# Kernel optimization log

Measured on AMD Instinct MI355X. Metric: run time of the kernel, lower is better.

Reference implementation:

```python
import jax, jax.numpy as jnp
import numpy as np

N = 50000      # nodes
E = 800000     # edges (before self loops)
D_IN = 128
HID = 64
HEADS = 8
D_OUT = 10


def setup_inputs() -> dict:
    key = jax.random.key(0)
    ks = jax.random.split(key, 16)
    sc = 0.05
    x = jax.random.normal(ks[0], (N, D_IN), dtype=jnp.float32)
    edge_index = jax.random.randint(ks[1], (2, E), 0, N, dtype=jnp.int64)
    return {
        "x": x,
        "edge_index": edge_index,
        "W1": jax.random.normal(ks[2], (HEADS * HID, D_IN), dtype=jnp.float32) * sc,
        "a1_src": jax.random.normal(ks[3], (HEADS, HID), dtype=jnp.float32) * sc,
        "a1_dst": jax.random.normal(ks[4], (HEADS, HID), dtype=jnp.float32) * sc,
        "b1": jnp.zeros((HEADS * HID,), jnp.float32),
        "W2": jax.random.normal(ks[5], (HID, HEADS * HID), dtype=jnp.float32) * sc,
        "a2_src": jax.random.normal(ks[6], (1, HID), dtype=jnp.float32) * sc,
        "a2_dst": jax.random.normal(ks[7], (1, HID), dtype=jnp.float32) * sc,
        "b2": jnp.zeros((HID,), jnp.float32),
        "W3": jax.random.normal(ks[8], (HID, HID), dtype=jnp.float32) * sc,
        "a3_src": jax.random.normal(ks[9], (1, HID), dtype=jnp.float32) * sc,
        "a3_dst": jax.random.normal(ks[10], (1, HID), dtype=jnp.float32) * sc,
        "b3": jnp.zeros((HID,), jnp.float32),
        "Wc": jax.random.normal(ks[11], (D_OUT, HID), dtype=jnp.float32) * sc,
        "bc": jnp.zeros((D_OUT,), jnp.float32),
    }


def gat_conv(x, src, dst, W, a_src, a_dst, b, concat):
    """PyG GATConv (eval mode, add_self_loops already applied to src/dst)."""
    heads, out_ch = a_src.shape
    n = x.shape[0]
    h = (x @ W.T).reshape(n, heads, out_ch)          # [N, H, C]
    a_s = jnp.einsum('nhc,hc->nh', h, a_src)          # [N, H]
    a_d = jnp.einsum('nhc,hc->nh', h, a_dst)          # [N, H]
    e = jax.nn.leaky_relu(a_s[src] + a_d[dst], 0.2)   # [Etot, H]
    # segment softmax over incoming edges of each destination node
    m = jax.ops.segment_max(e, dst, num_segments=n)
    ex = jnp.exp(e - m[dst])
    s = jax.ops.segment_sum(ex, dst, num_segments=n)
    alpha = ex / (s[dst] + 1e-16)                     # [Etot, H]
    out = jax.ops.segment_sum(h[src] * alpha[:, :, None], dst, num_segments=n)
    if concat:
        out = out.reshape(n, heads * out_ch)
    else:
        out = out.mean(axis=1)
    return out + b


def reference(x, edge_index, W1, a1_src, a1_dst, b1, W2, a2_src, a2_dst, b2,
              W3, a3_src, a3_dst, b3, Wc, bc):
    loops = jnp.arange(N, dtype=edge_index.dtype)
    src = jnp.concatenate([edge_index[0], loops])
    dst = jnp.concatenate([edge_index[1], loops])
    h = jax.nn.elu(gat_conv(x, src, dst, W1, a1_src, a1_dst, b1, True))
    h = jax.nn.elu(gat_conv(h, src, dst, W2, a2_src, a2_dst, b2, False))
    h = jax.nn.elu(gat_conv(h, src, dst, W3, a3_src, a3_dst, b3, False))
    return h @ Wc.T + bc
```

## Files before the change

### kernel.cpp

```cpp
#include <hip/hip_runtime.h>
#include <math.h>

#define N_NODES 50000
#define N_EDGES 800000
#define ETOT    (N_EDGES + N_NODES)
#define COL_CAP (ETOT + 3 * N_NODES + 64)

typedef short bf16x8 __attribute__((ext_vector_type(8)));
typedef float f32x4  __attribute__((ext_vector_type(4)));
typedef float f32x2  __attribute__((ext_vector_type(2)));

__device__ __forceinline__ float b2f(unsigned int u16) {
    return __uint_as_float(u16 << 16);
}
__device__ __forceinline__ unsigned short f2b(float f) {
    unsigned int u = __float_as_uint(f);
    u += 0x7fffu + ((u >> 16) & 1u);
    return (unsigned short)(u >> 16);
}

__global__ __launch_bounds__(256) void k_prep(const float* __restrict__ x,
                                              const float* __restrict__ w1,
                                              const float* __restrict__ w2,
                                              const float* __restrict__ w3,
                                              const float* __restrict__ a1s,
                                              const float* __restrict__ a1d,
                                              unsigned short* __restrict__ xb,
                                              unsigned short* __restrict__ o1,
                                              unsigned short* __restrict__ o2,
                                              unsigned short* __restrict__ o3,
                                              float* __restrict__ U,
                                              int* __restrict__ deg,
                                              int* __restrict__ flag) {
    int i = blockIdx.x * 256 + threadIdx.x;
    if (i < N_NODES) deg[i] = 0;
    if (i == 0) *flag = 0;
    if (blockIdx.x < 8) {
        int h = blockIdx.x;
        int which = threadIdx.x >> 7, k = threadIdx.x & 127;
        const float* av = which ? a1d : a1s;
        float acc = 0.f;
        for (int c = 0; c < 64; ++c)
            acc += av[h * 64 + c] * w1[(size_t)(h * 64 + c) * 128 + k];
        U[(which * 8 + h) * 128 + k] = acc;
    }
    if (i < 512 * 128 / 4) {
        float4 v = ((const float4*)w1)[i];
        ushort2* o = (ushort2*)(o1 + i * 4);
        o[0] = make_ushort2(f2b(v.x), f2b(v.y));
        o[1] = make_ushort2(f2b(v.z), f2b(v.w));
    }
    if (i < 64 * 512 / 4) {
        float4 v = ((const float4*)w2)[i];
        ushort2* o = (ushort2*)(o2 + i * 4);
        o[0] = make_ushort2(f2b(v.x), f2b(v.y));
        o[1] = make_ushort2(f2b(v.z), f2b(v.w));
    }
    if (i < 64 * 64 / 4) {
        float4 v = ((const float4*)w3)[i];
        ushort2* o = (ushort2*)(o3 + i * 4);
        o[0] = make_ushort2(f2b(v.x), f2b(v.y));
        o[1] = make_ushort2(f2b(v.z), f2b(v.w));
    }
    if (i < N_NODES * 128 / 8) {
        const float4* xp = (const float4*)x + (size_t)i * 2;
        float4 v0 = xp[0], v1 = xp[1];
        unsigned int u0 = (unsigned int)f2b(v0.x) | ((unsigned int)f2b(v0.y) << 16);
        unsigned int u1 = (unsigned int)f2b(v0.z) | ((unsigned int)f2b(v0.w) << 16);
        unsigned int u2 = (unsigned int)f2b(v1.x) | ((unsigned int)f2b(v1.y) << 16);
        unsigned int u3 = (unsigned int)f2b(v1.z) | ((unsigned int)f2b(v1.w) << 16);
        *(uint4*)(xb + (size_t)i * 8) = make_uint4(u0, u1, u2, u3);
    }
}

__global__ __launch_bounds__(256) void k_attn(const unsigned short* __restrict__ xb,
                                              const float* __restrict__ U,
                                              float* __restrict__ asrc,
                                              float* __restrict__ adst) {
    __shared__ float sU[16 * 132];
    __shared__ unsigned short sX[16 * 136];
    int t = threadIdx.x;
    for (int i = t; i < 2048; i += 256) sU[(i >> 7) * 132 + (i & 127)] = U[i];
    int n0 = blockIdx.x * 16;
    {
        int r = t >> 4, c = (t & 15) * 8;
        *(uint4*)&sX[r * 136 + c] = *(const uint4*)(xb + (size_t)(n0 + r) * 128 + c);
    }
    __syncthreads();
    int nl = t >> 4, o = t & 15;
    const unsigned short* xr = sX + nl * 136;
    const float* ur = sU + o * 132;
    float acc = 0.f;
#pragma unroll 8
    for (int k2 = 0; k2 < 128; ++k2) acc += b2f(xr[k2]) * ur[k2];
    int n = n0 + nl;
    if (o < 8) asrc[n * 8 + o] = acc;
    else       adst[n * 8 + (o - 8)] = acc;
}

__global__ void k_detect(const int* __restrict__ idx, int* __restrict__ flag) {
    int i = blockIdx.x * blockDim.x + threadIdx.x;
    int v = idx[2 * i + 1];
    unsigned long long any = __ballot(v != 0);
    if ((threadIdx.x & 63) == 0 && any) atomicOr(flag, 1);
}

__device__ __forceinline__ int edge_src(const int* idx, int e, int is32) {
    return is32 ? idx[e] : idx[2 * e];
}
__device__ __forceinline__ int edge_dst(const int* idx, int e, int is32) {
    return is32 ? idx[N_EDGES + e] : idx[2 * (N_EDGES + e)];
}

__global__ void k_degree(const int* __restrict__ idx, const int* __restrict__ flag,
                         int* __restrict__ deg) {
    int e = blockIdx.x * blockDim.x + threadIdx.x;
    if (e >= ETOT) return;
    int is32 = *flag;
    int d = (e < N_EDGES) ? edge_dst(idx, e, is32) : (e - N_EDGES);
    atomicAdd(&deg[d], 1);
}

__global__ __launch_bounds__(256) void k_scan1(const int* __restrict__ deg,
                                               int* __restrict__ rowptr,
                                               int* __restrict__ bsum) {
    __shared__ int sd[256];
    int t = threadIdx.x;
    int i = blockIdx.x * 256 + t;
    int v = (i < N_NODES) ? ((deg[i] + 3) & ~3) : 0;
    sd[t] = v;
    __syncthreads();
#pragma unroll
    for (int off = 1; off < 256; off <<= 1) {
        int a = (t >= off) ? sd[t - off] : 0;
        __syncthreads();
        sd[t] += a;
        __syncthreads();
    }
    if (i < N_NODES) rowptr[i] = sd[t] - v;
    if (t == 255) bsum[blockIdx.x] = sd[255];
}

__global__ __launch_bounds__(256) void k_scan2(int* __restrict__ bsum,
                                               int* __restrict__ boff,
                                               int* __restrict__ rowptr,
                                               int nb) {
    __shared__ int sd[256];
    int t = threadIdx.x;
    int v = (t < nb) ? bsum[t] : 0;
    sd[t] = v;
    __syncthreads();
#pragma unroll
    for (int off = 1; off < 256; off <<= 1) {
        int a = (t >= off) ? sd[t - off] : 0;
        __syncthreads();
        sd[t] += a;
        __syncthreads();
    }
    boff[t] = sd[t] - v;
    if (t == 255) rowptr[N_NODES] = sd[255];
}

__global__ __launch_bounds__(256) void k_scan3(int* __restrict__ rowptr,
                                               const int* __restrict__ boff,
                                               const int* __restrict__ deg,
                                               int* __restrict__ cursor,
                                               int* __restrict__ col) {
    int i = blockIdx.x * 256 + threadIdx.x;
    if (i == 0) {
        int tot = rowptr[N_NODES];
        for (int q = 0; q < 48; ++q) col[tot + q] = 0;
    }
    if (i >= N_NODES) return;
    int r = rowptr[i] + boff[blockIdx.x];
    rowptr[i] = r;
    cursor[i] = r;
    int d = deg[i];
    int pd = (d + 3) & ~3;
    for (int p = r + d; p < r + pd; ++p) col[p] = 0;
}

__global__ void k_scatter(const int* __restrict__ idx, const int* __restrict__ flag,
                          int* __restrict__ cursor, int* __restrict__ col) {
    int e = blockIdx.x * blockDim.x + threadIdx.x;
    if (e >= ETOT) return;
    int is32 = *flag;
    int s, d;
    if (e < N_EDGES) { s = edge_src(idx, e, is32); d = edge_dst(idx, e, is32); }
    else             { s = d = e - N_EDGES; }
    int pos = atomicAdd(&cursor[d], 1);
    col[pos] = s;
}

__device__ __forceinline__ void aggx_slot(int idx, int rem, float tt, unsigned int xx,
                                          float adn, float& ssum, f32x2* acc) {
    float e = tt + adn;
    e = fmaxf(e, 0.2f * e);
    float ex = __expf(e);
    ex = (idx < rem) ? ex : 0.f;
    ssum += ex;
    float fx = __uint_as_float(xx << 16);
    float fy = __uint_as_float(xx & 0xffff0000u);
    int exi = __float_as_int(ex);
#pragma unroll
    for (int hh = 0; hh < 8; ++hh) {
        float wh = __int_as_float(__builtin_amdgcn_readlane(exi, hh << 3));
        acc[hh].x = fmaf(fx, wh, acc[hh].x);
        acc[hh].y = fmaf(fy, wh, acc[hh].y);
    }
}

__global__ __launch_bounds__(256) void k_aggx(const unsigned short* __restrict__ xb,
                                              const float* __restrict__ asrc,
                                              const float* __restrict__ adst,
                                              const int* __restrict__ rowptr,
                                              const int* __restrict__ degv,
                                              const int* __restrict__ col,
                                              unsigned short* __restrict__ aggX) {
    int n = blockIdx.x * 4 + (threadIdx.x >> 6);
    if (n >= N_NODES) return;
    int l = threadIdx.x & 63;
    int j = l >> 3;
    unsigned lx2 = (unsigned)(l << 1);
    int start = rowptr[n];
    int end   = start + degv[n];
    float adn = adst[((unsigned)n << 3) + (unsigned)j];

    float ssum = 0.f;
    f32x2 acc[8];
#pragma unroll
    for (int hh = 0; hh < 8; ++hh) acc[hh] = (f32x2){0.f, 0.f};

    float tA0, tA1, tA2, tA3, tB0, tB1, tB2, tB3;
    unsigned int xA0, xA1, xA2, xA3, xB0, xB1, xB2, xB3;
    int4 cA, cB;

#define GATHX(c, T0, T1, T2, T3, X0, X1, X2, X3)                              \
    T0 = asrc[(((unsigned)(c).x) << 3) + (unsigned)j];                        \
    T1 = asrc[(((unsigned)(c).y) << 3) + (unsigned)j];                        \
    T2 = asrc[(((unsigned)(c).z) << 3) + (unsigned)j];                        \
    T3 = asrc[(((unsigned)(c).w) << 3) + (unsigned)j];                        \
    X0 = *(const unsigned int*)(xb + (((unsigned)(c).x) << 7) + lx2);         \
    X1 = *(const unsigned int*)(xb + (((unsigned)(c).y) << 7) + lx2);         \
    X2 = *(const unsigned int*)(xb + (((unsigned)(c).z) << 7) + lx2);         \
    X3 = *(const unsigned int*)(xb + (((unsigned)(c).w) << 7) + lx2);

    int k = start;
    cA = *(const int4*)(col + k);
    cB = *(const int4*)(col + k + 4);
    GATHX(cA, tA0, tA1, tA2, tA3, xA0, xA1, xA2, xA3);
    for (;;) {
        bool hasB = (k + 4 < end);
        if (hasB) {
            GATHX(cB, tB0, tB1, tB2, tB3, xB0, xB1, xB2, xB3);
            cA = *(const int4*)(col + k + 8);
        }
        {
            int rem = end - k;
            aggx_slot(0, rem, tA0, xA0, adn, ssum, acc);
            aggx_slot(1, rem, tA1, xA1, adn, ssum, acc);
            aggx_slot(2, rem, tA2, xA2, adn, ssum, acc);
            aggx_slot(3, rem, tA3, xA3, adn, ssum, acc);
        }
        k += 4;
        if (!hasB) break;
        bool hasA = (k + 4 < end);
        if (hasA) {
            GATHX(cA, tA0, tA1, tA2, tA3, xA0, xA1, xA2, xA3);
            cB = *(const int4*)(col + k + 8);
        }
        {
            int rem = end - k;
            aggx_slot(0, rem, tB0, xB0, adn, ssum, acc);
            aggx_slot(1, rem, tB1, xB1, adn, ssum, acc);
            aggx_slot(2, rem, tB2, xB2, adn, ssum, acc);
            aggx_slot(3, rem, tB3, xB3, adn, ssum, acc);
        }
        k += 4;
        if (!hasA) break;
    }
#undef GATHX

    size_t base = (size_t)n * 1024 + lx2;
#pragma unroll
    for (int hh = 0; hh < 8; ++hh) {
        float sh = __int_as_float(__builtin_amdgcn_readlane(__float_as_int(ssum), hh << 3));
        float iv = 1.f / (sh + 1e-16f);
        unsigned int lo = f2b(acc[hh].x * iv);
        unsigned int hi = f2b(acc[hh].y * iv);
        *(unsigned int*)(aggX + base + hh * 128) = lo | (hi << 16);
    }
}

__global__ __launch_bounds__(512, 4) void k_gemm12(const unsigned short* __restrict__ aggX,
                                                   const unsigned short* __restrict__ W1b,
                                                   const float* __restrict__ b1,
                                                   const unsigned short* __restrict__ W2b,
                                                   const float* __restrict__ a2s,
                                                   const float* __restrict__ a2d,
                                                   unsigned short* __restrict__ h2,
                                                   float* __restrict__ asb,
                                                   float* __restrict__ adb) {
    __shared__ unsigned short X2s[64 * 520];
    __shared__ float red_s[8][16];
    __shared__ float red_d[8][16];
    int t = threadIdx.x;
    int w = t >> 6, l = t & 63;
    int quad = l >> 4, lm = l & 15;
    int m0 = blockIdx.x * 64;

    {
        int h = w;
        f32x4 acc1[4][4];
#pragma unroll
        for (int rt = 0; rt < 4; ++rt)
#pragma unroll
            for (int ct = 0; ct < 4; ++ct) acc1[rt][ct] = (f32x4){0.f, 0.f, 0.f, 0.f};

#pragma unroll
        for (int k0 = 0; k0 < 4; ++k0) {
            bf16x8 af[4];
#pragma unroll
            for (int rt = 0; rt < 4; ++rt) {
                int m = m0 + rt * 16 + lm;
                uint4 au = make_uint4(0, 0, 0, 0);
                if (m < N_NODES)
                    au = *(const uint4*)(aggX + (size_t)m * 1024 + h * 128 + k0 * 32 + quad * 8);
                af[rt] = *(bf16x8*)&au;
            }
#pragma unroll
            for (int ct = 0; ct < 4; ++ct) {
                uint4 bu = *(const uint4*)(W1b + (size_t)(h * 64 + ct * 16 + lm) * 128 + k0 * 32 + quad * 8);
                bf16x8 bf_ = *(bf16x8*)&bu;
#pragma unroll
                for (int rt = 0; rt < 4; ++rt)
                    acc1[rt][ct] = __builtin_amdgcn_mfma_f32_16x16x32_bf16(af[rt], bf_, acc1[rt][ct], 0, 0, 0);
            }
        }
#pragma unroll
        for (int ct = 0; ct < 4; ++ct) {
            float bcol = b1[h * 64 + ct * 16 + lm];
#pragma unroll
            for (int rt = 0; rt < 4; ++rt)
#pragma unroll
                for (int g = 0; g < 4; ++g) {
                    float v = acc1[rt][ct][g] + bcol;
                    v = (v > 0.f) ? v : expm1f(v);
                    X2s[(rt * 16 + quad * 4 + g) * 520 + h * 64 + ct * 16 + lm] = f2b(v);
                }
        }
    }
    __syncthreads();

    int rt2 = w >> 1;
    int ct0 = (w & 1) * 2, ct1 = ct0 + 1;
    f32x4 acc2a = (f32x4){0.f, 0.f, 0.f, 0.f};
    f32x4 acc2b = (f32x4){0.f, 0.f, 0.f, 0.f};
#pragma unroll 4
    for (int k0 = 0; k0 < 512; k0 += 32) {
        bf16x8 af = *(const bf16x8*)&X2s[(rt2 * 16 + lm) * 520 + k0 + quad * 8];
        uint4 b0 = *(const uint4*)(W2b + (size_t)(ct0 * 16 + lm) * 512 + k0 + quad * 8);
        uint4 b1u = *(const uint4*)(W2b + (size_t)(ct1 * 16 + lm) * 512 + k0 + quad * 8);
        acc2a = __builtin_amdgcn_mfma_f32_16x16x32_bf16(af, *(bf16x8*)&b0, acc2a, 0, 0, 0);
        acc2b = __builtin_amdgcn_mfma_f32_16x16x32_bf16(af, *(bf16x8*)&b1u, acc2b, 0, 0, 0);
    }

#pragma unroll
    for (int g = 0; g < 4; ++g) {
        int m = m0 + rt2 * 16 + quad * 4 + g;
        if (m < N_NODES) {
            h2[(size_t)m * 64 + ct0 * 16 + lm] = f2b(acc2a[g]);
            h2[(size_t)m * 64 + ct1 * 16 + lm] = f2b(acc2b[g]);
        }
    }

    {
        float as0 = a2s[ct0 * 16 + lm], ad0 = a2d[ct0 * 16 + lm];
        float as1 = a2s[ct1 * 16 + lm], ad1 = a2d[ct1 * 16 + lm];
#pragma unroll
        for (int g = 0; g < 4; ++g) {
            float vs = acc2a[g] * as0 + acc2b[g] * as1;
            float vd = acc2a[g] * ad0 + acc2b[g] * ad1;
#pragma unroll
            for (int off = 1; off < 16; off <<= 1) {
                vs += __shfl_xor(vs, off);
                vd += __shfl_xor(vd, off);
            }
            if (lm == 0) {
                red_s[w][quad * 4 + g] = vs;
                red_d[w][quad * 4 + g] = vd;
            }
        }
    }
    __syncthreads();
    if (t < 64) {
        int rt = t >> 4, rr = t & 15;
        float vs = red_s[2 * rt][rr] + red_s[2 * rt + 1][rr];
        float vd = red_d[2 * rt][rr] + red_d[2 * rt + 1][rr];
        int m = m0 + t;
        if (m < N_NODES) {
            asb[m] = vs;
            adb[m] = vd;
        }
    }
}

__global__ __launch_bounds__(256) void k_gemm(const unsigned short* __restrict__ Ab,
                                              const unsigned short* __restrict__ W,
                                              unsigned short* __restrict__ C,
                                              const float* __restrict__ a_src,
                                              const float* __restrict__ a_dst,
                                              float* __restrict__ asb,
                                              float* __restrict__ adb,
                                              int M, int K, int Nout) {
    __shared__ unsigned short As[64 * 40];
    __shared__ unsigned short Bs[64 * 40];
    __shared__ float red_s[4][64];
    __shared__ float red_d[4][64];
    int t = threadIdx.x;
    int w = t >> 6, l = t & 63;
    int quad = l >> 4, lm = l & 15;
    int m0 = blockIdx.y * 64, n0 = blockIdx.x * 64;
    int lr = t >> 2;
    int lc = (t & 3) * 8;

    f32x4 acc[4];
#pragma unroll
    for (int r = 0; r < 4; ++r) acc[r] = (f32x4){0.f, 0.f, 0.f, 0.f};

    for (int k0 = 0; k0 < K; k0 += 32) {
        int m = m0 + lr;
        uint4 av = make_uint4(0, 0, 0, 0);
        if (m < M) av = *(const uint4*)(Ab + (size_t)m * K + k0 + lc);
        *(uint4*)&As[lr * 40 + lc] = av;
        uint4 bv = *(const uint4*)(W + (size_t)(n0 + lr) * K + k0 + lc);
        *(uint4*)&Bs[lr * 40 + lc] = bv;
        __syncthreads();

        bf16x8 bfrag = *(const bf16x8*)&Bs[(w * 16 + lm) * 40 + quad * 8];
#pragma unroll
        for (int r = 0; r < 4; ++r) {
            bf16x8 afrag = *(const bf16x8*)&As[(r * 16 + lm) * 40 + quad * 8];
            acc[r] = __builtin_amdgcn_mfma_f32_16x16x32_bf16(afrag, bfrag, acc[r], 0, 0, 0);
        }
        __syncthreads();
    }

#pragma unroll
    for (int r = 0; r < 4; ++r)
#pragma unroll
        for (int g = 0; g < 4; ++g) {
            int m = m0 + r * 16 + quad * 4 + g;
            if (m < M) C[(size_t)m * Nout + n0 + w * 16 + lm] = f2b(acc[r][g]);
        }

    float as = a_src[w * 16 + lm];
    float ad = a_dst[w * 16 + lm];
#pragma unroll
    for (int r = 0; r < 4; ++r) {
#pragma unroll
        for (int g = 0; g < 4; ++g) {
            float vs = acc[r][g] * as;
            float vd = acc[r][g] * ad;
#pragma unroll
            for (int off = 1; off < 16; off <<= 1) {
                vs += __shfl_xor(vs, off);
                vd += __shfl_xor(vd, off);
            }
            if (lm == 0) {
                red_s[w][r * 16 + quad * 4 + g] = vs;
                red_d[w][r * 16 + quad * 4 + g] = vd;
            }
        }
    }
    __syncthreads();
    if (t < 64) {
        float vs = red_s[0][t] + red_s[1][t] + red_s[2][t] + red_s[3][t];
        float vd = red_d[0][t] + red_d[1][t] + red_d[2][t] + red_d[3][t];
        int m = m0 + t;
        if (m < M) {
            asb[m] = vs;
            adb[m] = vd;
        }
    }
}

__global__ __launch_bounds__(256) void k_agg1(const unsigned short* __restrict__ h,
                                              const float* __restrict__ asrc,
                                              const float* __restrict__ adst,
                                              const int* __restrict__ rowptr,
                                              const int* __restrict__ degv,
                                              const int* __restrict__ col,
                                              const float* __restrict__ bias,
                                              unsigned short* __restrict__ out) {
    int n = blockIdx.x * 4 + (threadIdx.x >> 6);
    if (n >= N_NODES) return;
    int l = threadIdx.x & 63;
    int start = rowptr[n];
    int end   = start + degv[n];
    float adn = adst[n];

    float ssum = 0.f, o = 0.f;
    float tA0, tA1, tA2, tA3, tB0, tB1, tB2, tB3;
    unsigned short qA0, qA1, qA2, qA3, qB0, qB1, qB2, qB3;
    int4 cA, cB;

#define GATH1(c, T0, T1, T2, T3, Q0, Q1, Q2, Q3)                              \
    T0 = asrc[(unsigned)(c).x];                                               \
    T1 = asrc[(unsigned)(c).y];                                               \
    T2 = asrc[(unsigned)(c).z];                                               \
    T3 = asrc[(unsigned)(c).w];                                               \
    Q0 = h[(((unsigned)(c).x) << 6) + (unsigned)l];                           \
    Q1 = h[(((unsigned)(c).y) << 6) + (unsigned)l];                           \
    Q2 = h[(((unsigned)(c).z) << 6) + (unsigned)l];                           \
    Q3 = h[(((unsigned)(c).w) << 6) + (unsigned)l];

#define ASLOT1(IDX, TT, QQ, rem)                                              \
    {                                                                         \
        float e = TT + adn;                                                   \
        e = fmaxf(e, 0.2f * e);                                               \
        float ex = __expf(e);                                                 \
        ex = ((IDX) < (rem)) ? ex : 0.f;                                      \
        ssum += ex;                                                           \
        o += ex * b2f(QQ);                                                    \
    }

    int k = start;
    cA = *(const int4*)(col + k);
    cB = *(const int4*)(col + k + 4);
    GATH1(cA, tA0, tA1, tA2, tA3, qA0, qA1, qA2, qA3);
    for (;;) {
        bool hasB = (k + 4 < end);
        if (hasB) {
            GATH1(cB, tB0, tB1, tB2, tB3, qB0, qB1, qB2, qB3);
            cA = *(const int4*)(col + k + 8);
        }
        {
            int rem = end - k;
            ASLOT1(0, tA0, qA0, rem);
            ASLOT1(1, tA1, qA1, rem);
            ASLOT1(2, tA2, qA2, rem);
            ASLOT1(3, tA3, qA3, rem);
        }
        k += 4;
        if (!hasB) break;
        bool hasA = (k + 4 < end);
        if (hasA) {
            GATH1(cA, tA0, tA1, tA2, tA3, qA0, qA1, qA2, qA3);
            cB = *(const int4*)(col + k + 8);
        }
        {
            int rem = end - k;
            ASLOT1(0, tB0, qB0, rem);
            ASLOT1(1, tB1, qB1, rem);
            ASLOT1(2, tB2, qB2, rem);
            ASLOT1(3, tB3, qB3, rem);
        }
        k += 4;
        if (!hasA) break;
    }
#undef GATH1
#undef ASLOT1

    float v = o / (ssum + 1e-16f) + bias[l];
    v = (v > 0.f) ? v : expm1f(v);
    out[(size_t)n * 64 + l] = f2b(v);
}

__global__ __launch_bounds__(256) void k_classifier(const unsigned short* __restrict__ h,
                                                    const float* __restrict__ Wc,
                                                    const float* __restrict__ bc,
                                                    float* __restrict__ out) {
    __shared__ float sW[640];
    for (int i = threadIdx.x; i < 640; i += blockDim.x) sW[i] = Wc[i];
    __syncthreads();
    int idx = blockIdx.x * blockDim.x + threadIdx.x;
    if (idx >= N_NODES * 10) return;
    int n = idx / 10, d = idx - n * 10;
    const unsigned short* hr = h + (size_t)n * 64;
    const float* wr = sW + d * 64;
    float acc = 0.f;
#pragma unroll
    for (int c = 0; c < 64; ++c) acc += b2f(hr[c]) * wr[c];
    out[idx] = acc + bc[d];
}

extern "C" void kernel_launch(void* const* d_in, const int* in_sizes, int n_in,
                              void* d_out, int out_size, void* d_ws, size_t ws_size,
                              hipStream_t stream) {
    const float* x    = (const float*)d_in[0];
    const int*   eidx = (const int*)  d_in[1];
    const float* W1   = (const float*)d_in[2];
    const float* a1s  = (const float*)d_in[3];
    const float* a1d  = (const float*)d_in[4];
    const float* b1   = (const float*)d_in[5];
    const float* W2   = (const float*)d_in[6];
    const float* a2s  = (const float*)d_in[7];
    const float* a2d  = (const float*)d_in[8];
    const float* b2   = (const float*)d_in[9];
    const float* W3   = (const float*)d_in[10];
    const float* a3s  = (const float*)d_in[11];
    const float* a3d  = (const float*)d_in[12];
    const float* b3   = (const float*)d_in[13];
    const float* Wc   = (const float*)d_in[14];
    const float* bc   = (const float*)d_in[15];
    float* out = (float*)d_out;

    float* asbuf = (float*)d_ws;
    float* adbuf = asbuf + (size_t)N_NODES * 8;
    unsigned short* aggX = (unsigned short*)(adbuf + (size_t)N_NODES * 8);
    unsigned short* h2  = aggX + (size_t)N_NODES * 1024;
    unsigned short* x3  = h2  + (size_t)N_NODES * 64;
    unsigned short* h3  = x3  + (size_t)N_NODES * 64;
    unsigned short* x4  = h3  + (size_t)N_NODES * 64;
    unsigned short* xb  = x4  + (size_t)N_NODES * 64;
    unsigned short* W1b = xb  + (size_t)N_NODES * 128;
    unsigned short* W2b = W1b + 512 * 128;
    unsigned short* W3b = W2b + 64 * 512;
    float* U    = (float*)(W3b + 64 * 64);
    int* ibase  = (int*)(U + 16 * 128);
    int* deg    = ibase;
    int* flag   = deg + N_NODES;
    int* rowptr = flag + 1;
    int* cursor = rowptr + N_NODES + 1;
    int* bsum   = cursor + N_NODES;
    int* boff   = bsum + 256;
    int* col    = boff + 256;

    dim3 blk(256);
    const int SCAN_BLOCKS = (N_NODES + 255) / 256;
    const int PREP_BLOCKS = (N_NODES * 128 / 8 + 255) / 256;

    k_prep<<<PREP_BLOCKS, blk, 0, stream>>>(x, W1, W2, W3, a1s, a1d,
                                            xb, W1b, W2b, W3b, U, deg, flag);
    k_attn<<<N_NODES / 16, blk, 0, stream>>>(xb, U, asbuf, adbuf);

    k_detect<<<32, blk, 0, stream>>>(eidx, flag);
    k_degree<<<(ETOT + 255) / 256, blk, 0, stream>>>(eidx, flag, deg);
    k_scan1<<<SCAN_BLOCKS, blk, 0, stream>>>(deg, rowptr, bsum);
    k_scan2<<<1, blk, 0, stream>>>(bsum, boff, rowptr, SCAN_BLOCKS);
    k_scan3<<<SCAN_BLOCKS, blk, 0, stream>>>(rowptr, boff, deg, cursor, col);
    k_scatter<<<(ETOT + 255) / 256, blk, 0, stream>>>(eidx, flag, cursor, col);

    int mblocks = (N_NODES + 63) / 64;
    int nblocks = N_NODES / 4;

    k_aggx<<<nblocks, blk, 0, stream>>>(xb, asbuf, adbuf, rowptr, deg, col, aggX);

    k_gemm12<<<mblocks, dim3(512), 0, stream>>>(aggX, W1b, b1, W2b, a2s, a2d,
                                                h2, asbuf, adbuf);

    k_agg1<<<nblocks, blk, 0, stream>>>(h2, asbuf, adbuf, rowptr, deg, col, b2, x3);

    k_gemm<<<dim3(1, mblocks), blk, 0, stream>>>(x3, W3b, h3,
                                                 a3s, a3d, asbuf, adbuf,
                                                 N_NODES, 64, 64);
    k_agg1<<<nblocks, blk, 0, stream>>>(h3, asbuf, adbuf, rowptr, deg, col, b3, x4);

    k_classifier<<<(N_NODES * 10 + 255) / 256, blk, 0, stream>>>(x4, Wc, bc, out);
}
```

Measured before the change: 436.9 us.

## Halve gemm12 row tile and split agg1 edges across lane groups

k_gemm12 now processes 32 rows per block instead of 64. This halves shared memory and accumulators, raises the occupancy hint to 8, and gives each wave one 16x16 output tile in the second GEMM with a four-way reduction of attention scores. k_agg1 is restructured so each group of 16 lanes handles a different edge and loads 4 features as a ushort4, instead of every lane walking all edges for one feature. Partial sums are then combined with cross-group shuffles. The aim is to cut per-lane serial edge latency and improve memory parallelism, at the cost of extra shuffles and more gemm blocks reloading the weights.

```diff
diff --git a/kernel.cpp b/kernel.cpp
--- a/kernel.cpp
+++ b/kernel.cpp
@@ -292,7 +292,7 @@
     }
 }
 
-__global__ __launch_bounds__(512, 4) void k_gemm12(const unsigned short* __restrict__ aggX,
+__global__ __launch_bounds__(512, 8) void k_gemm12(const unsigned short* __restrict__ aggX,
                                                    const unsigned short* __restrict__ W1b,
                                                    const float* __restrict__ b1,
                                                    const unsigned short* __restrict__ W2b,
@@ -301,27 +301,27 @@
                                                    unsigned short* __restrict__ h2,
                                                    float* __restrict__ asb,
                                                    float* __restrict__ adb) {
-    __shared__ unsigned short X2s[64 * 520];
+    __shared__ unsigned short X2s[32 * 520];
     __shared__ float red_s[8][16];
     __shared__ float red_d[8][16];
     int t = threadIdx.x;
     int w = t >> 6, l = t & 63;
     int quad = l >> 4, lm = l & 15;
-    int m0 = blockIdx.x * 64;
+    int m0 = blockIdx.x * 32;
 
     {
         int h = w;
-        f32x4 acc1[4][4];
-#pragma unroll
-        for (int rt = 0; rt < 4; ++rt)
+        f32x4 acc1[2][4];
+#pragma unroll
+        for (int rt = 0; rt < 2; ++rt)
 #pragma unroll
             for (int ct = 0; ct < 4; ++ct) acc1[rt][ct] = (f32x4){0.f, 0.f, 0.f, 0.f};
 
 #pragma unroll
         for (int k0 = 0; k0 < 4; ++k0) {
-            bf16x8 af[4];
-#pragma unroll
-            for (int rt = 0; rt < 4; ++rt) {
+            bf16x8 af[2];
+#pragma unroll
+            for (int rt = 0; rt < 2; ++rt) {
                 int m = m0 + rt * 16 + lm;
                 uint4 au = make_uint4(0, 0, 0, 0);
                 if (m < N_NODES)
@@ -333,7 +333,7 @@
                 uint4 bu = *(const uint4*)(W1b + (size_t)(h * 64 + ct * 16 + lm) * 128 + k0 * 32 + quad * 8);
                 bf16x8 bf_ = *(bf16x8*)&bu;
 #pragma unroll
-                for (int rt = 0; rt < 4; ++rt)
+                for (int rt = 0; rt < 2; ++rt)
                     acc1[rt][ct] = __builtin_amdgcn_mfma_f32_16x16x32_bf16(af[rt], bf_, acc1[rt][ct], 0, 0, 0);
             }
         }
@@ -341,7 +341,7 @@
         for (int ct = 0; ct < 4; ++ct) {
             float bcol = b1[h * 64 + ct * 16 + lm];
 #pragma unroll
-            for (int rt = 0; rt < 4; ++rt)
+            for (int rt = 0; rt < 2; ++rt)
 #pragma unroll
                 for (int g = 0; g < 4; ++g) {
                     float v = acc1[rt][ct][g] + bcol;
@@ -352,35 +352,28 @@
     }
     __syncthreads();
 
-    int rt2 = w >> 1;
-    int ct0 = (w & 1) * 2, ct1 = ct0 + 1;
-    f32x4 acc2a = (f32x4){0.f, 0.f, 0.f, 0.f};
-    f32x4 acc2b = (f32x4){0.f, 0.f, 0.f, 0.f};
+    int rt2 = w & 1;
+    int ct2 = w >> 1;
+    f32x4 acc2 = (f32x4){0.f, 0.f, 0.f, 0.f};
 #pragma unroll 4
     for (int k0 = 0; k0 < 512; k0 += 32) {
         bf16x8 af = *(const bf16x8*)&X2s[(rt2 * 16 + lm) * 520 + k0 + quad * 8];
-        uint4 b0 = *(const uint4*)(W2b + (size_t)(ct0 * 16 + lm) * 512 + k0 + quad * 8);
-        uint4 b1u = *(const uint4*)(W2b + (size_t)(ct1 * 16 + lm) * 512 + k0 + quad * 8);
-        acc2a = __builtin_amdgcn_mfma_f32_16x16x32_bf16(af, *(bf16x8*)&b0, acc2a, 0, 0, 0);
-        acc2b = __builtin_amdgcn_mfma_f32_16x16x32_bf16(af, *(bf16x8*)&b1u, acc2b, 0, 0, 0);
+        uint4 bu = *(const uint4*)(W2b + (size_t)(ct2 * 16 + lm) * 512 + k0 + quad * 8);
+        acc2 = __builtin_amdgcn_mfma_f32_16x16x32_bf16(af, *(bf16x8*)&bu, acc2, 0, 0, 0);
     }
 
 #pragma unroll
     for (int g = 0; g < 4; ++g) {
         int m = m0 + rt2 * 16 + quad * 4 + g;
-        if (m < N_NODES) {
-            h2[(size_t)m * 64 + ct0 * 16 + lm] = f2b(acc2a[g]);
-            h2[(size_t)m * 64 + ct1 * 16 + lm] = f2b(acc2b[g]);
-        }
+        if (m < N_NODES) h2[(size_t)m * 64 + ct2 * 16 + lm] = f2b(acc2[g]);
     }
 
     {
-        float as0 = a2s[ct0 * 16 + lm], ad0 = a2d[ct0 * 16 + lm];
-        float as1 = a2s[ct1 * 16 + lm], ad1 = a2d[ct1 * 16 + lm];
+        float as = a2s[ct2 * 16 + lm], ad = a2d[ct2 * 16 + lm];
 #pragma unroll
         for (int g = 0; g < 4; ++g) {
-            float vs = acc2a[g] * as0 + acc2b[g] * as1;
-            float vd = acc2a[g] * ad0 + acc2b[g] * ad1;
+            float vs = acc2[g] * as;
+            float vd = acc2[g] * ad;
 #pragma unroll
             for (int off = 1; off < 16; off <<= 1) {
                 vs += __shfl_xor(vs, off);
@@ -393,10 +386,10 @@
         }
     }
     __syncthreads();
-    if (t < 64) {
+    if (t < 32) {
         int rt = t >> 4, rr = t & 15;
-        float vs = red_s[2 * rt][rr] + red_s[2 * rt + 1][rr];
-        float vd = red_d[2 * rt][rr] + red_d[2 * rt + 1][rr];
+        float vs = red_s[rt][rr] + red_s[rt + 2][rr] + red_s[rt + 4][rr] + red_s[rt + 6][rr];
+        float vd = red_d[rt][rr] + red_d[rt + 2][rr] + red_d[rt + 4][rr] + red_d[rt + 6][rr];
         int m = m0 + t;
         if (m < N_NODES) {
             asb[m] = vs;
@@ -496,75 +489,77 @@
     int n = blockIdx.x * 4 + (threadIdx.x >> 6);
     if (n >= N_NODES) return;
     int l = threadIdx.x & 63;
+    int g = l >> 4;
+    int i = l & 15;
+    unsigned ci = (unsigned)(i << 2);
     int start = rowptr[n];
     int end   = start + degv[n];
     float adn = adst[n];
 
-    float ssum = 0.f, o = 0.f;
-    float tA0, tA1, tA2, tA3, tB0, tB1, tB2, tB3;
-    unsigned short qA0, qA1, qA2, qA3, qB0, qB1, qB2, qB3;
-    int4 cA, cB;
-
-#define GATH1(c, T0, T1, T2, T3, Q0, Q1, Q2, Q3)                              \
-    T0 = asrc[(unsigned)(c).x];                                               \
-    T1 = asrc[(unsigned)(c).y];                                               \
-    T2 = asrc[(unsigned)(c).z];                                               \
-    T3 = asrc[(unsigned)(c).w];                                               \
-    Q0 = h[(((unsigned)(c).x) << 6) + (unsigned)l];                           \
-    Q1 = h[(((unsigned)(c).y) << 6) + (unsigned)l];                           \
-    Q2 = h[(((unsigned)(c).z) << 6) + (unsigned)l];                           \
-    Q3 = h[(((unsigned)(c).w) << 6) + (unsigned)l];
-
-#define ASLOT1(IDX, TT, QQ, rem)                                              \
+    float ssum = 0.f;
+    f32x4 o4 = (f32x4){0.f, 0.f, 0.f, 0.f};
+
+    int sA, sB;
+    float tA, tB;
+    ushort4 hA, hB;
+
+#define AGG1_ACC(TT, HH, rem)                                                 \
     {                                                                         \
         float e = TT + adn;                                                   \
         e = fmaxf(e, 0.2f * e);                                               \
         float ex = __expf(e);                                                 \
-        ex = ((IDX) < (rem)) ? ex : 0.f;                                      \
+        ex = (g < (rem)) ? ex : 0.f;                                          \
         ssum += ex;                                                           \
-        o += ex * b2f(QQ);                                                    \
+        o4[0] = fmaf(ex, b2f((HH).x), o4[0]);                                 \
+        o4[1] = fmaf(ex, b2f((HH).y), o4[1]);                                 \
+        o4[2] = fmaf(ex, b2f((HH).z), o4[2]);                                 \
+        o4[3] = fmaf(ex, b2f((HH).w), o4[3]);                                 \
     }
 
     int k = start;
-    cA = *(const int4*)(col + k);
-    cB = *(const int4*)(col + k + 4);
-    GATH1(cA, tA0, tA1, tA2, tA3, qA0, qA1, qA2, qA3);
+    sA = col[k + g];
+    tA = asrc[sA];
+    hA = *(const ushort4*)(h + (((unsigned)sA) << 6) + ci);
     for (;;) {
         bool hasB = (k + 4 < end);
         if (hasB) {
-            GATH1(cB, tB0, tB1, tB2, tB3, qB0, qB1, qB2, qB3);
-            cA = *(const int4*)(col + k + 8);
-        }
-        {
-            int rem = end - k;
-            ASLOT1(0, tA0, qA0, rem);
-            ASLOT1(1, tA1, qA1, rem);
-            ASLOT1(2, tA2, qA2, rem);
-            ASLOT1(3, tA3, qA3, rem);
-        }
+            sB = col[k + 4 + g];
+            tB = asrc[sB];
+            hB = *(const ushort4*)(h + (((unsigned)sB) << 6) + ci);
+        }
+        AGG1_ACC(tA, hA, end - k);
         k += 4;
         if (!hasB) break;
         bool hasA = (k + 4 < end);
         if (hasA) {
-            GATH1(cA, tA0, tA1, tA2, tA3, qA0, qA1, qA2, qA3);
-            cB = *(const int4*)(col + k + 8);
-        }
-        {
-            int rem = end - k;
-            ASLOT1(0, tB0, qB0, rem);
-            ASLOT1(1, tB1, qB1, rem);
-            ASLOT1(2, tB2, qB2, rem);
-            ASLOT1(3, tB3, qB3, rem);
-        }
+            sA = col[k + 4 + g];
+            tA = asrc[sA];
+            hA = *(const ushort4*)(h + (((unsigned)sA) << 6) + ci);
+        }
+        AGG1_ACC(tB, hB, end - k);
         k += 4;
         if (!hasA) break;
     }
-#undef GATH1
-#undef ASLOT1
-
-    float v = o / (ssum + 1e-16f) + bias[l];
-    v = (v > 0.f) ? v : expm1f(v);
-    out[(size_t)n * 64 + l] = f2b(v);
+#undef AGG1_ACC
+
+    ssum += __shfl_xor(ssum, 16);
+    ssum += __shfl_xor(ssum, 32);
+#pragma unroll
+    for (int c = 0; c < 4; ++c) {
+        o4[c] += __shfl_xor(o4[c], 16);
+        o4[c] += __shfl_xor(o4[c], 32);
+    }
+
+    if (g == 0) {
+        float inv = 1.f / (ssum + 1e-16f);
+        float4 bv = *(const float4*)(bias + ci);
+        float v0 = o4[0] * inv + bv.x; v0 = (v0 > 0.f) ? v0 : expm1f(v0);
+        float v1 = o4[1] * inv + bv.y; v1 = (v1 > 0.f) ? v1 : expm1f(v1);
+        float v2 = o4[2] * inv + bv.z; v2 = (v2 > 0.f) ? v2 : expm1f(v2);
+        float v3 = o4[3] * inv + bv.w; v3 = (v3 > 0.f) ? v3 : expm1f(v3);
+        ushort4 ov = make_ushort4(f2b(v0), f2b(v1), f2b(v2), f2b(v3));
+        *(ushort4*)(out + (size_t)n * 64 + ci) = ov;
+    }
 }
 
 __global__ __launch_bounds__(256) void k_classifier(const unsigned short* __restrict__ h,
@@ -642,13 +637,14 @@
     k_scan3<<<SCAN_BLOCKS, blk, 0, stream>>>(rowptr, boff, deg, cursor, col);
     k_scatter<<<(ETOT + 255) / 256, blk, 0, stream>>>(eidx, flag, cursor, col);
 
-    int mblocks = (N_NODES + 63) / 64;
-    int nblocks = N_NODES / 4;
+    int mblocks   = (N_NODES + 63) / 64;
+    int m32blocks = (N_NODES + 31) / 32;
+    int nblocks   = N_NODES / 4;
 
     k_aggx<<<nblocks, blk, 0, stream>>>(xb, asbuf, adbuf, rowptr, deg, col, aggX);
 
-    k_gemm12<<<mblocks, dim3(512), 0, stream>>>(aggX, W1b, b1, W2b, a2s, a2d,
-                                                h2, asbuf, adbuf);
+    k_gemm12<<<m32blocks, dim3(512), 0, stream>>>(aggX, W1b, b1, W2b, a2s, a2d,
+                                                  h2, asbuf, adbuf);
 
     k_agg1<<<nblocks, blk, 0, stream>>>(h2, asbuf, adbuf, rowptr, deg, col, b2, x3);
 
```

New measurement: 459.8 us. 1.05x slower.
